# Performance work log

Measured on AMD Instinct MI355X. Metric: run time of the kernel, lower is better.

## Reference

```python
import jax, jax.numpy as jnp
import numpy as np

TAU = 0.02
B, C, H, W = 8, 64, 256, 256


def setup_inputs() -> dict:
    key = jax.random.key(0)
    k1, k2, k3, k4, k5 = jax.random.split(key, 5)
    x = jax.random.normal(k1, (B, C, H, W), dtype=jnp.float32)
    # learned per-channel parameters (theta_a initialized near -4.0 as in the module,
    # small noise added so gradients/behavior are non-degenerate)
    theta_a = -4.0 + 0.1 * jax.random.normal(k2, (1, C, 1, 1), dtype=jnp.float32)
    theta_bx = 0.1 * jax.random.normal(k3, (1, C, 1, 1), dtype=jnp.float32)
    theta_by = 0.1 * jax.random.normal(k4, (1, C, 1, 1), dtype=jnp.float32)
    theta_c = 0.1 * jax.random.normal(k5, (1, C, 1, 1), dtype=jnp.float32)
    # base grid in normalized [-1,1] coords (align_corners=True convention)
    gy, gx = jnp.meshgrid(jnp.linspace(-1.0, 1.0, H, dtype=jnp.float32),
                          jnp.linspace(-1.0, 1.0, W, dtype=jnp.float32), indexing='ij')
    return {"x": x, "theta_a": theta_a, "theta_bx": theta_bx, "theta_by": theta_by,
            "theta_c": theta_c, "base_gx": gx, "base_gy": gy}


def _bilinear_shift_sample(x, base_gx, base_gy, sx, sy):
    """Bilinear grid_sample with border padding, align_corners=True,
    where the grid is base_grid shifted by a per-channel constant (sx, sy).
    x: [B,C,H,W]; base_gx/base_gy: [H,W]; sx, sy: [C] normalized shifts.
    Returns [B,C,H,W]."""
    gx = base_gx[None, :, :] + sx[:, None, None]          # [C,H,W]
    gy = base_gy[None, :, :] + sy[:, None, None]          # [C,H,W]
    # normalized -> pixel coords (align_corners=True), border padding = clamp
    px = jnp.clip((gx + 1.0) * 0.5 * (W - 1), 0.0, float(W - 1))
    py = jnp.clip((gy + 1.0) * 0.5 * (H - 1), 0.0, float(H - 1))
    x0f = jnp.floor(px)
    y0f = jnp.floor(py)
    wx = px - x0f                                          # [C,H,W]
    wy = py - y0f
    x0 = x0f.astype(jnp.int32)
    y0 = y0f.astype(jnp.int32)
    x1 = jnp.minimum(x0 + 1, W - 1)
    y1 = jnp.minimum(y0 + 1, H - 1)
    cidx = jnp.arange(C)[:, None, None]                    # [C,1,1]
    v00 = x[:, cidx, y0, x0]                               # [B,C,H,W]
    v01 = x[:, cidx, y0, x1]
    v10 = x[:, cidx, y1, x0]
    v11 = x[:, cidx, y1, x1]
    return (1.0 - wy) * ((1.0 - wx) * v00 + wx * v01) + wy * ((1.0 - wx) * v10 + wx * v11)


def reference(x, theta_a, theta_bx, theta_by, theta_c, base_gx, base_gy):
    a = jax.nn.softplus(theta_a)                           # [1,C,1,1]
    s = jnp.sqrt(a * TAU + 1e-8).reshape(C)                # diffusion shift per channel
    dx = (theta_bx * TAU).reshape(C)                       # drift shift per channel
    dy = (theta_by * TAU).reshape(C)
    u_px = _bilinear_shift_sample(x, base_gx, base_gy, s + dx, dy)
    u_nx = _bilinear_shift_sample(x, base_gx, base_gy, -s + dx, dy)
    u_py = _bilinear_shift_sample(x, base_gx, base_gy, dx, s + dy)
    u_ny = _bilinear_shift_sample(x, base_gx, base_gy, dx, -s + dy)
    evolution = 0.25 * (u_px + u_nx + u_py + u_ny)
    return evolution + TAU * theta_c * x
```

## Files before the change

kernel.cpp:

```cpp
#include <hip/hip_runtime.h>

#define TAU 0.02f

constexpr int Bc = 8, Cc = 64, Hc = 256, Wc = 256;
constexpr int R  = 16;
constexpr int NR = 24;

__device__ __forceinline__ void coordf(float g, float shift, int n,
                                       int& i0, int& i1, float& w) {
    float p = (g + shift + 1.0f) * (0.5f * (float)(n - 1));
    p = fminf(fmaxf(p, 0.0f), (float)(n - 1));
    float f = floorf(p);
    w  = p - f;
    i0 = (int)f;
    i1 = min(i0 + 1, n - 1);
}

__device__ __forceinline__ void coord_adj(float g, float shift, int n,
                                          int& m, float& w) {
    int i0, i1; float ww;
    coordf(g, shift, n, i0, i1, ww);
    const bool top = (i0 == n - 1);
    m = top ? n - 2 : i0;
    w = top ? 1.0f  : ww;
}

__device__ __forceinline__ float gy_of(int i) {
    return fmaf((float)i, 2.0f / 255.0f, -1.0f);
}

__device__ __forceinline__ float rdlane_f(float v, int lane) {
    return __int_as_float(__builtin_amdgcn_readlane(__float_as_int(v), lane));
}

__global__ __launch_bounds__(256, 6) void remizov_sten(
    const float* __restrict__ x,
    const float* __restrict__ th_a,
    const float* __restrict__ th_bx,
    const float* __restrict__ th_by,
    const float* __restrict__ th_c,
    const float* __restrict__ base_gx,
    const float* __restrict__ base_gy,
    float* __restrict__ out)
{
    __shared__ float tile[NR * Wc];

    const int j  = threadIdx.x;
    const int i0 = blockIdx.x * R;
    const int c  = blockIdx.y;
    const int b  = blockIdx.z;

    const float a  = log1pf(expf(th_a[c]));
    const float s  = sqrtf(a * TAU + 1e-8f);
    const float dx = th_bx[c] * TAU;
    const float dy = th_by[c] * TAU;
    const float tc = th_c[c]  * TAU;

    const int lane16 = j & 15;
    int   m_yc, m_yp, m_yn;
    float m_wc, m_wp, m_wn;
    {
        const float gyr = gy_of(i0 + lane16);
        coord_adj(gyr,      dy, Hc, m_yc, m_wc);
        coord_adj(gyr,  s + dy, Hc, m_yp, m_wp);
        coord_adj(gyr, -s + dy, Hc, m_yn, m_wn);
    }

    int rlo = min(i0, min(min(__builtin_amdgcn_readlane(m_yc, 0),
                              __builtin_amdgcn_readlane(m_yp, 0)),
                              __builtin_amdgcn_readlane(m_yn, 0)));
    int rhi = max(i0 + R - 1, max(max(__builtin_amdgcn_readlane(m_yc, 15),
                                      __builtin_amdgcn_readlane(m_yp, 15)),
                                      __builtin_amdgcn_readlane(m_yn, 15)) + 1);
    const int nrows = rhi - rlo + 1;

    const float gxv = base_gx[j];
    int xp, xn, xc; float wxp, wxn, wxc;
    coord_adj(gxv,  s + dx, Wc, xp, wxp);
    coord_adj(gxv, -s + dx, Wc, xn, wxn);
    coord_adj(gxv,      dx, Wc, xc, wxc);

    const size_t plane = (size_t)(b * Cc + c) * (size_t)(Hc * Wc);
    float* __restrict__ dst = out + plane + (size_t)i0 * Wc + j;

    if (nrows > NR) {
        const float* __restrict__ P = x + plane;
        for (int r = 0; r < R; ++r) {
            const float gyr = gy_of(i0 + r);
            int yc, yp, yn; float wyc, wyp, wyn;
            coord_adj(gyr,      dy, Hc, yc, wyc);
            coord_adj(gyr,  s + dy, Hc, yp, wyp);
            coord_adj(gyr, -s + dy, Hc, yn, wyn);
            auto bilg = [&](int y0, float wy, int x0, float wx) -> float {
                const float* r0 = P + y0 * Wc;
                const float* r1 = r0 + Wc;
                float t0 = r0[x0] + wx * (r0[x0 + 1] - r0[x0]);
                float t1 = r1[x0] + wx * (r1[x0 + 1] - r1[x0]);
                return t0 + wy * (t1 - t0);
            };
            float v0 = bilg(yc, wyc, xp, wxp);
            float v1 = bilg(yc, wyc, xn, wxn);
            float v2 = bilg(yp, wyp, xc, wxc);
            float v3 = bilg(yn, wyn, xc, wxc);
            float xv = P[(i0 + r) * Wc + j];
            dst[r * Wc] = 0.25f * (v0 + v1 + v2 + v3) + tc * xv;
        }
        return;
    }

    {
        const float* __restrict__ src = x + plane + (size_t)rlo * Wc;
        const int total = nrows * Wc;
        for (int e = j * 4; e < total; e += 256 * 4) {
            *reinterpret_cast<float4*>(&tile[e]) =
                *reinterpret_cast<const float4*>(src + e);
        }
    }
    __syncthreads();

    const int acr = __builtin_amdgcn_readlane(m_yc, 8) - (i0 + 8);
    const int apr = __builtin_amdgcn_readlane(m_yp, 8) - (i0 + 8);
    const int anr = __builtin_amdgcn_readlane(m_yn, 8) - (i0 + 8);
    const float wc = rdlane_f(m_wc, 8);
    const float wp = rdlane_f(m_wp, 8);
    const float wn = rdlane_f(m_wn, 8);

    bool ok = (m_yc == i0 + lane16 + acr) &&
              (m_yp == i0 + lane16 + apr) &&
              (m_yn == i0 + lane16 + anr);
    const unsigned long long mask = __ballot(ok);

    if (mask == 0xFFFFFFFFFFFFFFFFull) {
        const int icp = (i0 + acr - rlo) * Wc + xp;
        const int icn = (i0 + acr - rlo) * Wc + xn;
        const int ipp = (i0 + apr - rlo) * Wc + xc;
        const int inn = (i0 + anr - rlo) * Wc + xc;
        const int ixx = (i0       - rlo) * Wc + j;

        auto lerp2 = [&](int idx, float w) -> float {
            float t0 = tile[idx], t1 = tile[idx + 1];
            return t0 + w * (t1 - t0);
        };

        float Sc0 = lerp2(icp,      wxp) + lerp2(icn,      wxn);
        float Sc1 = lerp2(icp + Wc, wxp) + lerp2(icn + Wc, wxn);
        float Wp0 = lerp2(ipp,      wxc);
        float Wp1 = lerp2(ipp + Wc, wxc);
        float Wn0 = lerp2(inn,      wxc);
        float Wn1 = lerp2(inn + Wc, wxc);

#pragma unroll
        for (int r = 0; r < R; ++r) {
            float v01 = Sc0 + wc * (Sc1 - Sc0);
            float v2  = Wp0 + wp * (Wp1 - Wp0);
            float v3  = Wn0 + wn * (Wn1 - Wn0);
            float xv  = tile[ixx + r * Wc];
            dst[(size_t)(r << 8)] = 0.25f * (v01 + v2 + v3) + tc * xv;
            if (r < R - 1) {
                const int adv = (r + 2) * Wc;
                Sc0 = Sc1;
                Sc1 = lerp2(icp + adv, wxp) + lerp2(icn + adv, wxn);
                Wp0 = Wp1;
                Wp1 = lerp2(ipp + adv, wxc);
                Wn0 = Wn1;
                Wn1 = lerp2(inn + adv, wxc);
            }
        }
    } else {
        auto ldH = [&](int row, int xm, float wx) -> float {
            row = min(max(row, rlo), rhi);
            const int base = (row - rlo) << 8;
            float t0 = tile[base + xm], t1 = tile[base + xm + 1];
            return t0 + wx * (t1 - t0);
        };
        auto ldS = [&](int row) -> float {
            return ldH(row, xp, wxp) + ldH(row, xn, wxn);
        };
        const int xvbase = (i0 - rlo) * Wc + j;
        for (int r = 0; r < R; ++r) {
            const float gyr = gy_of(i0 + r);
            int yc, yp, yn; float wyc, wyp, wyn;
            coord_adj(gyr,      dy, Hc, yc, wyc);
            coord_adj(gyr,  s + dy, Hc, yp, wyp);
            coord_adj(gyr, -s + dy, Hc, yn, wyn);
            float v01 = (1.0f - wyc) * ldS(yc) + wyc * ldS(yc + 1);
            float v2  = (1.0f - wyp) * ldH(yp,     xc, wxc)
                      +         wyp  * ldH(yp + 1, xc, wxc);
            float v3  = (1.0f - wyn) * ldH(yn,     xc, wxc)
                      +         wyn  * ldH(yn + 1, xc, wxc);
            const float xv = tile[xvbase + (r << 8)];
            dst[(size_t)(r << 8)] = 0.25f * (v01 + v2 + v3) + tc * xv;
        }
    }
}

extern "C" void kernel_launch(void* const* d_in, const int* in_sizes, int n_in,
                              void* d_out, int out_size, void* d_ws, size_t ws_size,
                              hipStream_t stream)
{
    const float* x       = (const float*)d_in[0];
    const float* th_a    = (const float*)d_in[1];
    const float* th_bx   = (const float*)d_in[2];
    const float* th_by   = (const float*)d_in[3];
    const float* th_c    = (const float*)d_in[4];
    const float* base_gx = (const float*)d_in[5];
    const float* base_gy = (const float*)d_in[6];
    float* out = (float*)d_out;

    dim3 grid(Hc / R, Cc, Bc);
    dim3 block(Wc);
    remizov_sten<<<grid, block, 0, stream>>>(x, th_a, th_bx, th_by, th_c,
                                             base_gx, base_gy, out);
}
```

Measured before the change: 262.0 us.

## Drop LDS tile staging and read stencil taps directly from global memory

Removes the shared-memory tile, its cooperative float4 fill, and the __syncthreads barrier, so every bilinear tap and the x term is loaded directly from global memory and relies on L1/L2 caching. It also drops the separate fallback path used when the row span exceeded the tile and raises the occupancy hint in launch_bounds from 6 to 8. The goal is to remove the barrier stall and the LDS traffic and let more waves hide latency. In exchange, each element is now fetched several times through the vector cache (about 8 gathers plus one load per output), which adds cache pressure and more load instructions.

```diff
diff --git a/kernel.cpp b/kernel.cpp
--- a/kernel.cpp
+++ b/kernel.cpp
@@ -4,7 +4,6 @@
 
 constexpr int Bc = 8, Cc = 64, Hc = 256, Wc = 256;
 constexpr int R  = 16;
-constexpr int NR = 24;
 
 __device__ __forceinline__ void coordf(float g, float shift, int n,
                                        int& i0, int& i1, float& w) {
@@ -33,7 +32,7 @@
     return __int_as_float(__builtin_amdgcn_readlane(__float_as_int(v), lane));
 }
 
-__global__ __launch_bounds__(256, 6) void remizov_sten(
+__global__ __launch_bounds__(256, 8) void remizov_sten(
     const float* __restrict__ x,
     const float* __restrict__ th_a,
     const float* __restrict__ th_bx,
@@ -43,8 +42,6 @@
     const float* __restrict__ base_gy,
     float* __restrict__ out)
 {
-    __shared__ float tile[NR * Wc];
-
     const int j  = threadIdx.x;
     const int i0 = blockIdx.x * R;
     const int c  = blockIdx.y;
@@ -66,14 +63,6 @@
         coord_adj(gyr, -s + dy, Hc, m_yn, m_wn);
     }
 
-    int rlo = min(i0, min(min(__builtin_amdgcn_readlane(m_yc, 0),
-                              __builtin_amdgcn_readlane(m_yp, 0)),
-                              __builtin_amdgcn_readlane(m_yn, 0)));
-    int rhi = max(i0 + R - 1, max(max(__builtin_amdgcn_readlane(m_yc, 15),
-                                      __builtin_amdgcn_readlane(m_yp, 15)),
-                                      __builtin_amdgcn_readlane(m_yn, 15)) + 1);
-    const int nrows = rhi - rlo + 1;
-
     const float gxv = base_gx[j];
     int xp, xn, xc; float wxp, wxn, wxc;
     coord_adj(gxv,  s + dx, Wc, xp, wxp);
@@ -81,42 +70,8 @@
     coord_adj(gxv,      dx, Wc, xc, wxc);
 
     const size_t plane = (size_t)(b * Cc + c) * (size_t)(Hc * Wc);
+    const float* __restrict__ P = x + plane;
     float* __restrict__ dst = out + plane + (size_t)i0 * Wc + j;
-
-    if (nrows > NR) {
-        const float* __restrict__ P = x + plane;
-        for (int r = 0; r < R; ++r) {
-            const float gyr = gy_of(i0 + r);
-            int yc, yp, yn; float wyc, wyp, wyn;
-            coord_adj(gyr,      dy, Hc, yc, wyc);
-            coord_adj(gyr,  s + dy, Hc, yp, wyp);
-            coord_adj(gyr, -s + dy, Hc, yn, wyn);
-            auto bilg = [&](int y0, float wy, int x0, float wx) -> float {
-                const float* r0 = P + y0 * Wc;
-                const float* r1 = r0 + Wc;
-                float t0 = r0[x0] + wx * (r0[x0 + 1] - r0[x0]);
-                float t1 = r1[x0] + wx * (r1[x0 + 1] - r1[x0]);
-                return t0 + wy * (t1 - t0);
-            };
-            float v0 = bilg(yc, wyc, xp, wxp);
-            float v1 = bilg(yc, wyc, xn, wxn);
-            float v2 = bilg(yp, wyp, xc, wxc);
-            float v3 = bilg(yn, wyn, xc, wxc);
-            float xv = P[(i0 + r) * Wc + j];
-            dst[r * Wc] = 0.25f * (v0 + v1 + v2 + v3) + tc * xv;
-        }
-        return;
-    }
-
-    {
-        const float* __restrict__ src = x + plane + (size_t)rlo * Wc;
-        const int total = nrows * Wc;
-        for (int e = j * 4; e < total; e += 256 * 4) {
-            *reinterpret_cast<float4*>(&tile[e]) =
-                *reinterpret_cast<const float4*>(src + e);
-        }
-    }
-    __syncthreads();
 
     const int acr = __builtin_amdgcn_readlane(m_yc, 8) - (i0 + 8);
     const int apr = __builtin_amdgcn_readlane(m_yp, 8) - (i0 + 8);
@@ -125,58 +80,42 @@
     const float wp = rdlane_f(m_wp, 8);
     const float wn = rdlane_f(m_wn, 8);
 
-    bool ok = (m_yc == i0 + lane16 + acr) &&
-              (m_yp == i0 + lane16 + apr) &&
-              (m_yn == i0 + lane16 + anr);
-    const unsigned long long mask = __ballot(ok);
+    bool okc = (m_yc == i0 + lane16 + acr) &&
+               (m_yp == i0 + lane16 + apr) &&
+               (m_yn == i0 + lane16 + anr);
+    const unsigned long long mask = __ballot(okc);
+
+    auto ldS = [&](int y) -> float {
+        const float* rp = P + (size_t)y * Wc;
+        float a0 = rp[xp], a1 = rp[xp + 1];
+        float b0 = rp[xn], b1 = rp[xn + 1];
+        return (a0 + wxp * (a1 - a0)) + (b0 + wxn * (b1 - b0));
+    };
+    auto ldC = [&](int y) -> float {
+        const float* rp = P + (size_t)y * Wc;
+        float a0 = rp[xc], a1 = rp[xc + 1];
+        return a0 + wxc * (a1 - a0);
+    };
 
     if (mask == 0xFFFFFFFFFFFFFFFFull) {
-        const int icp = (i0 + acr - rlo) * Wc + xp;
-        const int icn = (i0 + acr - rlo) * Wc + xn;
-        const int ipp = (i0 + apr - rlo) * Wc + xc;
-        const int inn = (i0 + anr - rlo) * Wc + xc;
-        const int ixx = (i0       - rlo) * Wc + j;
-
-        auto lerp2 = [&](int idx, float w) -> float {
-            float t0 = tile[idx], t1 = tile[idx + 1];
-            return t0 + w * (t1 - t0);
-        };
-
-        float Sc0 = lerp2(icp,      wxp) + lerp2(icn,      wxn);
-        float Sc1 = lerp2(icp + Wc, wxp) + lerp2(icn + Wc, wxn);
-        float Wp0 = lerp2(ipp,      wxc);
-        float Wp1 = lerp2(ipp + Wc, wxc);
-        float Wn0 = lerp2(inn,      wxc);
-        float Wn1 = lerp2(inn + Wc, wxc);
+        float Sc0 = ldS(i0 + acr), Sc1 = ldS(i0 + acr + 1);
+        float Wp0 = ldC(i0 + apr), Wp1 = ldC(i0 + apr + 1);
+        float Wn0 = ldC(i0 + anr), Wn1 = ldC(i0 + anr + 1);
 
 #pragma unroll
         for (int r = 0; r < R; ++r) {
             float v01 = Sc0 + wc * (Sc1 - Sc0);
             float v2  = Wp0 + wp * (Wp1 - Wp0);
             float v3  = Wn0 + wn * (Wn1 - Wn0);
-            float xv  = tile[ixx + r * Wc];
+            float xv  = P[(size_t)(i0 + r) * Wc + j];
             dst[(size_t)(r << 8)] = 0.25f * (v01 + v2 + v3) + tc * xv;
             if (r < R - 1) {
-                const int adv = (r + 2) * Wc;
-                Sc0 = Sc1;
-                Sc1 = lerp2(icp + adv, wxp) + lerp2(icn + adv, wxn);
-                Wp0 = Wp1;
-                Wp1 = lerp2(ipp + adv, wxc);
-                Wn0 = Wn1;
-                Wn1 = lerp2(inn + adv, wxc);
+                Sc0 = Sc1; Sc1 = ldS(i0 + r + 2 + acr);
+                Wp0 = Wp1; Wp1 = ldC(i0 + r + 2 + apr);
+                Wn0 = Wn1; Wn1 = ldC(i0 + r + 2 + anr);
             }
         }
     } else {
-        auto ldH = [&](int row, int xm, float wx) -> float {
-            row = min(max(row, rlo), rhi);
-            const int base = (row - rlo) << 8;
-            float t0 = tile[base + xm], t1 = tile[base + xm + 1];
-            return t0 + wx * (t1 - t0);
-        };
-        auto ldS = [&](int row) -> float {
-            return ldH(row, xp, wxp) + ldH(row, xn, wxn);
-        };
-        const int xvbase = (i0 - rlo) * Wc + j;
         for (int r = 0; r < R; ++r) {
             const float gyr = gy_of(i0 + r);
             int yc, yp, yn; float wyc, wyp, wyn;
@@ -184,11 +123,9 @@
             coord_adj(gyr,  s + dy, Hc, yp, wyp);
             coord_adj(gyr, -s + dy, Hc, yn, wyn);
             float v01 = (1.0f - wyc) * ldS(yc) + wyc * ldS(yc + 1);
-            float v2  = (1.0f - wyp) * ldH(yp,     xc, wxc)
-                      +         wyp  * ldH(yp + 1, xc, wxc);
-            float v3  = (1.0f - wyn) * ldH(yn,     xc, wxc)
-                      +         wyn  * ldH(yn + 1, xc, wxc);
-            const float xv = tile[xvbase + (r << 8)];
+            float v2  = (1.0f - wyp) * ldC(yp) + wyp * ldC(yp + 1);
+            float v3  = (1.0f - wyn) * ldC(yn) + wyn * ldC(yn + 1);
+            float xv  = P[(size_t)(i0 + r) * Wc + j];
             dst[(size_t)(r << 8)] = 0.25f * (v01 + v2 + v3) + tc * xv;
         }
     }
```

New measurement: 365.3 us. 39.4% more time.
